# Kernel tuning notes

Measured on AMD Instinct MI355X. Metric: run time of the kernel, lower is better.

Reference implementation:

```python
import jax, jax.numpy as jnp
import numpy as np

B, H, W, C = 4, 64, 64, 256
D = C // 8  # reduction_ratio = 8


def setup_inputs() -> dict:
    key = jax.random.key(0)
    ks = jax.random.split(key, 6)
    scale = 1.0 / np.sqrt(C)
    return {
        "x": jax.random.normal(ks[0], (B, H, W, C), dtype=jnp.float32),
        "Wf": jax.random.normal(ks[1], (C, D), dtype=jnp.float32) * scale,
        "Wg": jax.random.normal(ks[2], (C, D), dtype=jnp.float32) * scale,
        "Wh": jax.random.normal(ks[3], (C, D), dtype=jnp.float32) * scale,
        "Wv": jax.random.normal(ks[4], (D, C), dtype=jnp.float32) * (1.0 / np.sqrt(D)),
        "gamma": jax.random.normal(ks[5], (), dtype=jnp.float32),
    }


def reference(x, Wf, Wg, Wh, Wv, gamma):
    b, h, w, c = x.shape
    n = h * w
    xf = x.reshape(b, n, c)
    # 1x1 convs (no bias) == per-pixel matmuls over channels
    q = xf @ Wf  # [b, n, d]
    k = xf @ Wg  # [b, n, d]
    v = xf @ Wh  # [b, n, d]
    # beta[i, j] = k_i . q_j ; softmax over last (query) axis, unscaled
    beta = jax.nn.softmax(jnp.einsum('bnd,bmd->bnm', k, q), axis=-1)  # [b, n, n]
    o = jnp.einsum('bnm,bmd->bnd', beta, v)  # [b, n, d]
    o = o.reshape(b, h, w, -1) @ Wv  # output 1x1 conv -> [b, h, w, c]
    return gamma * o + x
```

## Files before the change

### kernel.cpp

```cpp
#include <hip/hip_runtime.h>
#include <hip/hip_bf16.h>
#include <stdint.h>


typedef __attribute__((ext_vector_type(8))) short bf16x8;
typedef __attribute__((ext_vector_type(4))) short bf16x4;
typedef __attribute__((ext_vector_type(4))) float f32x4;
typedef unsigned short ushort_t;

static __device__ __forceinline__ ushort_t f2bf(float f) {
    __hip_bfloat16 h = __float2bfloat16(f);
    return __builtin_bit_cast(ushort_t, h);
}
static __device__ __forceinline__ float bf2f(ushort_t u) {
    return __bfloat162float(__builtin_bit_cast(__hip_bfloat16, u));
}

static __device__ __forceinline__ f32x4 mfma16bf(bf16x4 a, bf16x4 b, f32x4 c) {
#if __has_builtin(__builtin_amdgcn_mfma_f32_16x16x16bf16_1k)
    return __builtin_amdgcn_mfma_f32_16x16x16bf16_1k(a, b, c, 0, 0, 0);
#else
    f32x4 d;
    asm("v_mfma_f32_16x16x16_bf16 %0, %1, %2, %3"
        : "=v"(d) : "v"(a), "v"(b), "v"(c));
    return d;
#endif
}

static __device__ __forceinline__ float fexp2(float x) {
#if __has_builtin(__builtin_amdgcn_exp2f)
    return __builtin_amdgcn_exp2f(x);
#else
    return exp2f(x);
#endif
}

#define NROWS 16384
#define NTOK  4096
#define QKS   40
#define LOG2E 1.44269504088896340736f

__global__ __launch_bounds__(256) void qkv_kernel(
    const float* __restrict__ x,
    const float* __restrict__ Wf, const float* __restrict__ Wg,
    const float* __restrict__ Wh,
    ushort_t* __restrict__ qh,
    ushort_t* __restrict__ kh, ushort_t* __restrict__ kl,
    ushort_t* __restrict__ vT)
{
    __shared__ __align__(16) ushort_t xh[32 * QKS];
    __shared__ __align__(16) ushort_t xl[32 * QKS];

    const int tid  = threadIdx.x;
    const int wave = tid >> 6;
    const int lane = tid & 63;
    const int ln15 = lane & 15;
    const int quad = lane >> 4;
    const int row0 = blockIdx.x * 32;
    const int rg     = wave & 1;
    const int cgbase = wave >> 1;
    const int r  = tid >> 3;
    const int pp = (tid & 7) * 4;

    f32x4 acc[3];
    #pragma unroll
    for (int ci = 0; ci < 3; ++ci) acc[ci] = (f32x4){0.f, 0.f, 0.f, 0.f};

    float4 xa = *reinterpret_cast<const float4*>(&x[(row0 + r) * 256 + pp]);

    for (int k0 = 0; k0 < 256; k0 += 32) {
        bf16x8 bh[3], bl[3];
        #pragma unroll
        for (int ci = 0; ci < 3; ++ci) {
            int cg = cgbase + ci * 2;
            const float* Wsrc = (cg < 2) ? Wf : (cg < 4) ? Wg : Wh;
            int c = (cg & 1) * 16 + ln15;
            ushort_t hv8[8], lv8[8];
            #pragma unroll
            for (int j = 0; j < 8; ++j) {
                float w = Wsrc[(k0 + quad * 8 + j) * 32 + c];
                ushort_t hi = f2bf(w);
                hv8[j] = hi;
                lv8[j] = f2bf(w - bf2f(hi));
            }
            bh[ci] = *reinterpret_cast<bf16x8*>(hv8);
            bl[ci] = *reinterpret_cast<bf16x8*>(lv8);
        }
        float fv[4];
        *reinterpret_cast<float4*>(fv) = xa;
        ushort_t hv[4], lv[4];
        #pragma unroll
        for (int j = 0; j < 4; ++j) {
            hv[j] = f2bf(fv[j]);
            lv[j] = f2bf(fv[j] - bf2f(hv[j]));
        }
        __syncthreads();
        *reinterpret_cast<uint2*>(&xh[r * QKS + pp]) = *reinterpret_cast<uint2*>(hv);
        *reinterpret_cast<uint2*>(&xl[r * QKS + pp]) = *reinterpret_cast<uint2*>(lv);
        __syncthreads();
        if (k0 < 224)
            xa = *reinterpret_cast<const float4*>(&x[(row0 + r) * 256 + k0 + 32 + pp]);

        const bf16x8 ah = *reinterpret_cast<const bf16x8*>(
            &xh[(rg * 16 + ln15) * QKS + quad * 8]);
        const bf16x8 al = *reinterpret_cast<const bf16x8*>(
            &xl[(rg * 16 + ln15) * QKS + quad * 8]);
        #pragma unroll
        for (int ci = 0; ci < 3; ++ci) {
            acc[ci] = __builtin_amdgcn_mfma_f32_16x16x32_bf16(ah, bh[ci], acc[ci], 0, 0, 0);
            acc[ci] = __builtin_amdgcn_mfma_f32_16x16x32_bf16(al, bh[ci], acc[ci], 0, 0, 0);
            acc[ci] = __builtin_amdgcn_mfma_f32_16x16x32_bf16(ah, bl[ci], acc[ci], 0, 0, 0);
        }
    }

    #pragma unroll
    for (int ci = 0; ci < 3; ++ci) {
        int cg = cgbase + ci * 2;
        int cc = (cg & 1) * 16 + ln15;
        int rowb = row0 + rg * 16 + quad * 4;
        if (cg < 2) {
            #pragma unroll
            for (int rr = 0; rr < 4; ++rr)
                qh[(rowb + rr) * 32 + cc] = f2bf(acc[ci][rr] * LOG2E);
        } else if (cg < 4) {
            #pragma unroll
            for (int rr = 0; rr < 4; ++rr) {
                float val = acc[ci][rr];
                ushort_t hi = f2bf(val);
                kh[(rowb + rr) * 32 + cc] = hi;
                kl[(rowb + rr) * 32 + cc] = f2bf(val - bf2f(hi));
            }
        } else {
            int bb = row0 >> 12;
            int m  = (row0 & 4095) + rg * 16 + quad * 4;
            ushort4 h4;
            h4.x = f2bf(acc[ci][0]);
            h4.y = f2bf(acc[ci][1]);
            h4.z = f2bf(acc[ci][2]);
            h4.w = f2bf(acc[ci][3]);
            *reinterpret_cast<ushort4*>(&vT[bb * 131072 + cc * 4096 + m]) = h4;
        }
    }
}

__global__ __launch_bounds__(512, 2) void attn_kernel(
    const ushort_t* __restrict__ qhg,
    const ushort_t* __restrict__ khg, const ushort_t* __restrict__ klg,
    const ushort_t* __restrict__ vT,
    const float* __restrict__ Wv, const float* __restrict__ x,
    const float* __restrict__ gamma, float* __restrict__ out)
{
    __shared__ float Ored[8][32][65];
    __shared__ float Lred[8][64];
    __shared__ float wv[8192];
    __shared__ float Os[64][33];
    __shared__ float linv[64];

    const int tid  = threadIdx.x;
    const int wave = tid >> 6;
    const int lane = tid & 63;
    const int ln15 = lane & 15;
    const int quad = lane >> 4;

    const int b    = blockIdx.x >> 6;
    const int n0   = (blockIdx.x & 63) * 64;
    const int base = b * NTOK;
    const int bb   = b * 131072;

    bf16x8 khf[4], klf[4];
    #pragma unroll
    for (int t = 0; t < 4; ++t) {
        khf[t] = *reinterpret_cast<const bf16x8*>(
            &khg[(base + n0 + t * 16 + ln15) * 32 + quad * 8]);
        klf[t] = *reinterpret_cast<const bf16x8*>(
            &klg[(base + n0 + t * 16 + ln15) * 32 + quad * 8]);
    }

    #pragma unroll
    for (int i = 0; i < 16; ++i) wv[tid + i * 512] = Wv[tid + i * 512];

    f32x4 accO[2][4];
    #pragma unroll
    for (int s01 = 0; s01 < 2; ++s01)
        #pragma unroll
        for (int t = 0; t < 4; ++t)
            accO[s01][t] = (f32x4){0.f, 0.f, 0.f, 0.f};
    float lacc[4] = {0.f, 0.f, 0.f, 0.f};

    const int mbase = wave * 16;
    const ushort_t* qp  = qhg + (size_t)(base + mbase + ln15) * 32 + quad * 8;
    const ushort_t* vp0 = vT + bb + ln15 * 4096 + mbase + quad * 4;
    const ushort_t* vp1 = vp0 + 16 * 4096;

    for (int it = 0; it < 32; ++it) {
        const bf16x8 qf  = *reinterpret_cast<const bf16x8*>(qp);
        const bf16x4 va0 = *reinterpret_cast<const bf16x4*>(vp0);
        const bf16x4 va1 = *reinterpret_cast<const bf16x4*>(vp1);
        qp  += 128 * 32;
        vp0 += 128;
        vp1 += 128;

        #pragma unroll
        for (int t = 0; t < 4; ++t) {
            f32x4 s = __builtin_amdgcn_mfma_f32_16x16x32_bf16(
                qf, khf[t], (f32x4){0.f, 0.f, 0.f, 0.f}, 0, 0, 0);
            s = __builtin_amdgcn_mfma_f32_16x16x32_bf16(qf, klf[t], s, 0, 0, 0);

            float p0 = fexp2(s[0]);
            float p1 = fexp2(s[1]);
            float p2 = fexp2(s[2]);
            float p3 = fexp2(s[3]);
            lacc[t] += (p0 + p1) + (p2 + p3);

            ushort_t pu[4];
            pu[0] = f2bf(p0);
            pu[1] = f2bf(p1);
            pu[2] = f2bf(p2);
            pu[3] = f2bf(p3);
            const bf16x4 pb = *reinterpret_cast<bf16x4*>(pu);

            accO[0][t] = mfma16bf(va0, pb, accO[0][t]);
            accO[1][t] = mfma16bf(va1, pb, accO[1][t]);
        }
    }

    #pragma unroll
    for (int s01 = 0; s01 < 2; ++s01)
        #pragma unroll
        for (int t = 0; t < 4; ++t)
            #pragma unroll
            for (int rr = 0; rr < 4; ++rr)
                Ored[wave][s01 * 16 + quad * 4 + rr][t * 16 + ln15] = accO[s01][t][rr];

    #pragma unroll
    for (int t = 0; t < 4; ++t) {
        float v = lacc[t];
        v += __shfl_xor(v, 16);
        v += __shfl_xor(v, 32);
        if (quad == 0) Lred[wave][t * 16 + ln15] = v;
    }
    __syncthreads();

    #pragma unroll
    for (int i = 0; i < 4; ++i) {
        int idx = i * 512 + tid;
        int d = idx & 31;
        int n = idx >> 5;
        float v = (Ored[0][d][n] + Ored[1][d][n]) + (Ored[2][d][n] + Ored[3][d][n])
                + (Ored[4][d][n] + Ored[5][d][n]) + (Ored[6][d][n] + Ored[7][d][n]);
        Os[n][d] = v;
    }
    if (tid < 64) {
        float s = (Lred[0][tid] + Lred[1][tid]) + (Lred[2][tid] + Lred[3][tid])
                + (Lred[4][tid] + Lred[5][tid]) + (Lred[6][tid] + Lred[7][tid]);
        linv[tid] = 1.0f / s;
    }
    __syncthreads();

    const float g  = gamma[0];
    const int   c  = tid & 255;
    const int   nh = (tid >> 8) * 32;
    const int rowb = base + n0 + nh;
    #pragma unroll
    for (int rc = 0; rc < 32; rc += 8) {
        float acc[8];
        #pragma unroll
        for (int rr = 0; rr < 8; ++rr) acc[rr] = 0.f;
        for (int d = 0; d < 32; ++d) {
            float wvd = wv[d * 256 + c];
            #pragma unroll
            for (int rr = 0; rr < 8; ++rr) acc[rr] += Os[nh + rc + rr][d] * wvd;
        }
        #pragma unroll
        for (int rr = 0; rr < 8; ++rr) {
            int row = rowb + rc + rr;
            out[row * 256 + c] = g * acc[rr] * linv[nh + rc + rr] + x[row * 256 + c];
        }
    }
}

extern "C" void kernel_launch(void* const* d_in, const int* in_sizes, int n_in,
                              void* d_out, int out_size, void* d_ws, size_t ws_size,
                              hipStream_t stream)
{
    const float* x     = (const float*)d_in[0];
    const float* Wf    = (const float*)d_in[1];
    const float* Wg    = (const float*)d_in[2];
    const float* Wh    = (const float*)d_in[3];
    const float* Wv    = (const float*)d_in[4];
    const float* gamma = (const float*)d_in[5];
    float* out = (float*)d_out;

    ushort_t* qh = (ushort_t*)d_ws;
    ushort_t* kh = qh + NROWS * 32;
    ushort_t* kl = kh + NROWS * 32;
    ushort_t* vT = kl + NROWS * 32;

    qkv_kernel<<<dim3(512), dim3(256), 0, stream>>>(x, Wf, Wg, Wh, qh, kh, kl, vT);
    attn_kernel<<<dim3(256), dim3(512), 0, stream>>>(qh, kh, kl, vT, Wv, x, gamma, out);
}
```

Baseline: 113.4 us.

## Split attention key range over 16 waves and prefetch next Q/V tiles

The attention kernel moves from 512 to 1024 threads per block. Each of the 16 waves now covers half as many query tiles, and the two groups of 8 waves combine their partial outputs and row sums in shared memory in two stages. The Q and V fragments for the next iteration are loaded before the current one is computed, to hide global load latency. The hi/lo bf16 split in the QKV kernel now takes the high half by bit truncation instead of a rounding conversion. The main risk is that the new launch bounds squeeze the register budget and cause spills, plus the extra barrier and read-modify-write reduction steps.

```diff
diff --git a/kernel.cpp b/kernel.cpp
--- a/kernel.cpp
+++ b/kernel.cpp
@@ -14,6 +14,12 @@
 }
 static __device__ __forceinline__ float bf2f(ushort_t u) {
     return __bfloat162float(__builtin_bit_cast(__hip_bfloat16, u));
+}
+static __device__ __forceinline__ void tsplit(float w, ushort_t& hi, ushort_t& lo) {
+    uint32_t b = __builtin_bit_cast(uint32_t, w);
+    hi = (ushort_t)(b >> 16);
+    float hf = __builtin_bit_cast(float, b & 0xFFFF0000u);
+    lo = f2bf(w - hf);
 }
 
 static __device__ __forceinline__ f32x4 mfma16bf(bf16x4 a, bf16x4 b, f32x4 c) {
@@ -79,9 +85,7 @@
             #pragma unroll
             for (int j = 0; j < 8; ++j) {
                 float w = Wsrc[(k0 + quad * 8 + j) * 32 + c];
-                ushort_t hi = f2bf(w);
-                hv8[j] = hi;
-                lv8[j] = f2bf(w - bf2f(hi));
+                tsplit(w, hv8[j], lv8[j]);
             }
             bh[ci] = *reinterpret_cast<bf16x8*>(hv8);
             bl[ci] = *reinterpret_cast<bf16x8*>(lv8);
@@ -90,10 +94,7 @@
         *reinterpret_cast<float4*>(fv) = xa;
         ushort_t hv[4], lv[4];
         #pragma unroll
-        for (int j = 0; j < 4; ++j) {
-            hv[j] = f2bf(fv[j]);
-            lv[j] = f2bf(fv[j] - bf2f(hv[j]));
-        }
+        for (int j = 0; j < 4; ++j) tsplit(fv[j], hv[j], lv[j]);
         __syncthreads();
         *reinterpret_cast<uint2*>(&xh[r * QKS + pp]) = *reinterpret_cast<uint2*>(hv);
         *reinterpret_cast<uint2*>(&xl[r * QKS + pp]) = *reinterpret_cast<uint2*>(lv);
@@ -125,10 +126,10 @@
         } else if (cg < 4) {
             #pragma unroll
             for (int rr = 0; rr < 4; ++rr) {
-                float val = acc[ci][rr];
-                ushort_t hi = f2bf(val);
+                ushort_t hi, lo;
+                tsplit(acc[ci][rr], hi, lo);
                 kh[(rowb + rr) * 32 + cc] = hi;
-                kl[(rowb + rr) * 32 + cc] = f2bf(val - bf2f(hi));
+                kl[(rowb + rr) * 32 + cc] = lo;
             }
         } else {
             int bb = row0 >> 12;
@@ -143,7 +144,7 @@
     }
 }
 
-__global__ __launch_bounds__(512, 2) void attn_kernel(
+__global__ __launch_bounds__(1024, 4) void attn_kernel(
     const ushort_t* __restrict__ qhg,
     const ushort_t* __restrict__ khg, const ushort_t* __restrict__ klg,
     const ushort_t* __restrict__ vT,
@@ -177,7 +178,7 @@
     }
 
     #pragma unroll
-    for (int i = 0; i < 16; ++i) wv[tid + i * 512] = Wv[tid + i * 512];
+    for (int i = 0; i < 8; ++i) wv[tid + i * 1024] = Wv[tid + i * 1024];
 
     f32x4 accO[2][4];
     #pragma unroll
@@ -192,13 +193,17 @@
     const ushort_t* vp0 = vT + bb + ln15 * 4096 + mbase + quad * 4;
     const ushort_t* vp1 = vp0 + 16 * 4096;
 
-    for (int it = 0; it < 32; ++it) {
-        const bf16x8 qf  = *reinterpret_cast<const bf16x8*>(qp);
-        const bf16x4 va0 = *reinterpret_cast<const bf16x4*>(vp0);
-        const bf16x4 va1 = *reinterpret_cast<const bf16x4*>(vp1);
-        qp  += 128 * 32;
-        vp0 += 128;
-        vp1 += 128;
+    bf16x8 qf  = *reinterpret_cast<const bf16x8*>(qp);
+    bf16x4 va0 = *reinterpret_cast<const bf16x4*>(vp0);
+    bf16x4 va1 = *reinterpret_cast<const bf16x4*>(vp1);
+
+    for (int it = 0; it < 16; ++it) {
+        qp  += 256 * 32;
+        vp0 += 256;
+        vp1 += 256;
+        bf16x8 nqf  = *reinterpret_cast<const bf16x8*>(qp);
+        bf16x4 nva0 = *reinterpret_cast<const bf16x4*>(vp0);
+        bf16x4 nva1 = *reinterpret_cast<const bf16x4*>(vp1);
 
         #pragma unroll
         for (int t = 0; t < 4; ++t) {
@@ -222,28 +227,50 @@
             accO[0][t] = mfma16bf(va0, pb, accO[0][t]);
             accO[1][t] = mfma16bf(va1, pb, accO[1][t]);
         }
-    }
-
-    #pragma unroll
-    for (int s01 = 0; s01 < 2; ++s01)
-        #pragma unroll
-        for (int t = 0; t < 4; ++t)
-            #pragma unroll
-            for (int rr = 0; rr < 4; ++rr)
-                Ored[wave][s01 * 16 + quad * 4 + rr][t * 16 + ln15] = accO[s01][t][rr];
-
+        qf = nqf; va0 = nva0; va1 = nva1;
+    }
+
+    float lr[4];
     #pragma unroll
     for (int t = 0; t < 4; ++t) {
         float v = lacc[t];
         v += __shfl_xor(v, 16);
         v += __shfl_xor(v, 32);
-        if (quad == 0) Lred[wave][t * 16 + ln15] = v;
+        lr[t] = v;
+    }
+    if (wave < 8) {
+        #pragma unroll
+        for (int s01 = 0; s01 < 2; ++s01)
+            #pragma unroll
+            for (int t = 0; t < 4; ++t)
+                #pragma unroll
+                for (int rr = 0; rr < 4; ++rr)
+                    Ored[wave][s01 * 16 + quad * 4 + rr][t * 16 + ln15] = accO[s01][t][rr];
+        if (quad == 0) {
+            #pragma unroll
+            for (int t = 0; t < 4; ++t) Lred[wave][t * 16 + ln15] = lr[t];
+        }
     }
     __syncthreads();
-
-    #pragma unroll
-    for (int i = 0; i < 4; ++i) {
-        int idx = i * 512 + tid;
+    if (wave >= 8) {
+        const int ws = wave - 8;
+        #pragma unroll
+        for (int s01 = 0; s01 < 2; ++s01)
+            #pragma unroll
+            for (int t = 0; t < 4; ++t)
+                #pragma unroll
+                for (int rr = 0; rr < 4; ++rr)
+                    Ored[ws][s01 * 16 + quad * 4 + rr][t * 16 + ln15] += accO[s01][t][rr];
+        if (quad == 0) {
+            #pragma unroll
+            for (int t = 0; t < 4; ++t) Lred[ws][t * 16 + ln15] += lr[t];
+        }
+    }
+    __syncthreads();
+
+    #pragma unroll
+    for (int i = 0; i < 2; ++i) {
+        int idx = i * 1024 + tid;
         int d = idx & 31;
         int n = idx >> 5;
         float v = (Ored[0][d][n] + Ored[1][d][n]) + (Ored[2][d][n] + Ored[3][d][n])
@@ -259,10 +286,10 @@
 
     const float g  = gamma[0];
     const int   c  = tid & 255;
-    const int   nh = (tid >> 8) * 32;
+    const int   nh = (tid >> 8) * 16;
     const int rowb = base + n0 + nh;
     #pragma unroll
-    for (int rc = 0; rc < 32; rc += 8) {
+    for (int rc = 0; rc < 16; rc += 8) {
         float acc[8];
         #pragma unroll
         for (int rr = 0; rr < 8; ++rr) acc[rr] = 0.f;
@@ -297,5 +324,5 @@
     ushort_t* vT = kl + NROWS * 32;
 
     qkv_kernel<<<dim3(512), dim3(256), 0, stream>>>(x, Wf, Wg, Wh, qh, kh, kl, vT);
-    attn_kernel<<<dim3(256), dim3(512), 0, stream>>>(qh, kh, kl, vT, Wv, x, gamma, out);
-}
+    attn_kernel<<<dim3(256), dim3(1024), 0, stream>>>(qh, kh, kl, vT, Wv, x, gamma, out);
+}
```

After: 112.3 us. Within noise of the previous version (-1.0%).
